# Kernel tuning notes

Measured on AMD Instinct MI355X. Metric: run time of the kernel, lower is better.

## Reference

```python
import jax, jax.numpy as jnp
import numpy as np
import math

HEADS = 8


def sinusoidal_pe_2d(C, H, W, dtype=jnp.float32):
    """Standard fixed 2D sinusoidal PE. Returns (C, H*W).
    First C/2 channels encode row (H) position, last C/2 encode column (W)."""
    half = C // 2
    div = jnp.exp(-math.log(10000.0) * jnp.arange(0, half, 2, dtype=dtype) / half)  # (half/2,)
    pos_h = jnp.arange(H, dtype=dtype)[:, None] * div[None, :]  # (H, half/2)
    pos_w = jnp.arange(W, dtype=dtype)[:, None] * div[None, :]  # (W, half/2)
    # interleave sin/cos along channel dim -> (H, half), (W, half)
    pe_h = jnp.stack([jnp.sin(pos_h), jnp.cos(pos_h)], axis=-1).reshape(H, half)
    pe_w = jnp.stack([jnp.sin(pos_w), jnp.cos(pos_w)], axis=-1).reshape(W, half)
    pe = jnp.concatenate([
        jnp.broadcast_to(pe_h.T[:, :, None], (half, H, W)),
        jnp.broadcast_to(pe_w.T[:, None, :], (half, H, W)),
    ], axis=0)  # (C, H, W)
    return pe.reshape(C, H * W)


def setup_inputs() -> dict:
    key = jax.random.key(0)
    k1, k2, k3, k4 = jax.random.split(key, 4)
    B, c_in, H, W = 16, 256, 64, 64
    c_out = 512
    s = 1.0 / math.sqrt(c_in)
    return {
        "x": jax.random.normal(k1, (B, c_in, H, W), dtype=jnp.float32),
        "Wq": jax.random.normal(k2, (c_out, c_in), dtype=jnp.float32) * s,
        "Wk": jax.random.normal(k3, (c_out, c_in), dtype=jnp.float32) * s,
        "Wv": jax.random.normal(k4, (c_out, c_in), dtype=jnp.float32) * s,
    }


def reference(x, Wq, Wk, Wv):
    B, C, H, W = x.shape
    M = H * W
    c_out = Wq.shape[0]
    heads = HEADS
    dh = c_out // heads
    scale = 1.0 / math.sqrt(dh)

    xf = x.reshape(B, C, M)
    # 1x1 convs (no bias) == channel matmuls
    q = jnp.einsum('oc,bcm->bom', Wq, xf).reshape(B, heads, dh, M)
    k = jnp.einsum('oc,bcm->bom', Wk, xf).reshape(B, heads, dh, M)
    v = jnp.einsum('oc,bcm->bom', Wv, xf).reshape(B, heads, dh, M)

    r = sinusoidal_pe_2d(c_out, H, W, dtype=x.dtype).reshape(1, heads, dh, M)
    q = (jax.nn.elu(q + r) + 1.0) * scale  # feature map phi(q)
    k = (jax.nn.elu(k) + 1.0) * scale      # feature map phi(k)

    KV = jnp.einsum('bhcm,bhdm->bhcd', k, v)          # (B,h,dh,dh)
    out = jnp.einsum('bhcd,bhcm->bhdm', KV, q)        # (B,h,dh,M)
    k_sum = k.sum(axis=-1)                            # (B,h,dh)
    denom = jnp.einsum('bhcm,bhc->bhm', q, k_sum)
    denom = jnp.maximum(denom, 1e-6)[:, :, None, :]   # (B,h,1,M)
    out = out / denom
    return out.reshape(B, c_out, H, W)
```

## Files before the change

### kernel.cpp

```cpp
#include <hip/hip_runtime.h>

#define NB   16
#define CIN  256
#define MM   4096
#define COUT 512
#define NH   8
#define DH   64
#define SCALE 0.125f

typedef __attribute__((ext_vector_type(8))) short bf16x8;
typedef __attribute__((ext_vector_type(4))) float f32x4;

#define PEH_OFF   0u
#define PEW_OFF   65536u
#define WQ_OFF    131072u
#define WKV_OFF   393216u
#define KVP_OFF   917504u
#define KSP_OFF   9306112u
#define AEXT_OFF  9437184u
#define XT_OFF    27787264u
#define WS_NEED   61341696ull

__device__ __forceinline__ unsigned short f2bf(float f) {
    unsigned int u = __float_as_uint(f);
    u = (u + 0x7FFFu + ((u >> 16) & 1u)) >> 16;
    return (unsigned short)u;
}
__device__ __forceinline__ float phi_elu(float x) {
    return (x >= 0.f ? x + 1.f : __expf(x)) * SCALE;
}
__device__ __forceinline__ void gload_lds16(const void* g, void* l) {
    __builtin_amdgcn_global_load_lds(
        (const __attribute__((address_space(1))) unsigned int*)g,
        (__attribute__((address_space(3))) unsigned int*)l, 16, 0, 0);
}

__global__ void k_prep(const float* __restrict__ Wq, const float* __restrict__ Wk,
                       const float* __restrict__ Wv, char* __restrict__ ws) {
    int idx = blockIdx.x * 256 + threadIdx.x;
    if (idx < 32768) {
        int which = idx >> 14;
        int r = idx & 16383;
        int c = r >> 6, pos = r & 63;
        float div = __expf(-logf(10000.f) * (float)(c >> 1) * (1.f / 128.f));
        float t = (float)pos * div;
        float v = (c & 1) ? cosf(t) : sinf(t);
        ((float*)(ws + (which ? PEW_OFF : PEH_OFF)))[r] = v;
        return;
    }
    idx -= 32768;
    if (idx < COUT * CIN) {
        ((unsigned short*)(ws + WQ_OFF))[idx] = f2bf(Wq[idx]);
        return;
    }
    idx -= COUT * CIN;
    if (idx < NH * 128 * CIN) {
        int h = idx >> 15;
        int r = idx & 32767;
        int row = r >> 8, c = r & 255;
        float v = (row < 64) ? Wk[(h * 64 + row) * CIN + c]
                             : Wv[(h * 64 + row - 64) * CIN + c];
        ((unsigned short*)(ws + WKV_OFF))[idx] = f2bf(v);
    }
}


__global__ __launch_bounds__(256) void k_xpose(const float* __restrict__ x, char* __restrict__ ws) {
    __shared__ unsigned short tile[64 * 64];
    int t = threadIdx.x;
    int gx = blockIdx.x;
    int ct = gx & 3, mt = (gx >> 2) & 63, b = gx >> 8;
    int m0 = mt * 64, c0 = ct * 64;
    const float* xb = x + ((size_t)b * CIN + c0) * MM + m0;
    int m4 = (t & 15) * 4;
    int cp0 = (t >> 4) * 2;
#pragma unroll
    for (int p = 0; p < 2; ++p) {
        int cp = cp0 + p * 32;
        float4 v0 = *(const float4*)(xb + (size_t)cp * MM + m4);
        float4 v1 = *(const float4*)(xb + (size_t)(cp + 1) * MM + m4);
        float a0[4] = {v0.x, v0.y, v0.z, v0.w};
        float a1[4] = {v1.x, v1.y, v1.z, v1.w};
#pragma unroll
        for (int i = 0; i < 4; ++i) {
            int m = m4 + i;
            unsigned pk = (unsigned)f2bf(a0[i]) | ((unsigned)f2bf(a1[i]) << 16);
            unsigned off = (unsigned)(m * 128) + (((unsigned)(cp * 2)) ^ ((unsigned)(m & 7) << 4));
            *(unsigned*)((char*)tile + off) = pk;
        }
    }
    __syncthreads();
    unsigned short* xt = (unsigned short*)(ws + XT_OFF) + ((size_t)b * MM + m0) * CIN + c0;
#pragma unroll
    for (int p = 0; p < 2; ++p) {
        int id = t + p * 256;
        int m = id >> 3, u = id & 7;
        unsigned off = (unsigned)(m * 128) + (((unsigned)(u ^ (m & 7))) << 4);
        *(bf16x8*)(xt + (size_t)m * CIN + u * 8) = *(const bf16x8*)((const char*)tile + off);
    }
}

__device__ __forceinline__ void stage_half(const unsigned short* __restrict__ tile_base, int h,
                                           unsigned short* __restrict__ buf, int l, int w) {
#pragma unroll
    for (int i = 0; i < 4; ++i) {
        int r0 = w * 16 + i * 4;
        int m = r0 + (l >> 4);
        unsigned u = (unsigned)(l & 15) ^ (unsigned)(m & 7);
        const char* g = (const char*)tile_base + m * 512 + h * 256 + u * 16;
        gload_lds16(g, (char*)buf + r0 * 256);
    }
}
__device__ __forceinline__ bf16x8 ldsBh(const unsigned short* buf, int n, int k) {
    unsigned off = (unsigned)(n * 256) + (((((unsigned)k) >> 3) ^ ((unsigned)n & 7)) << 4);
    return *(const bf16x8*)((const char*)buf + off);
}

__global__ __launch_bounds__(256) void k_kv4(const char* __restrict__ ws) {
    __shared__ unsigned short bufA[64 * 128];
    __shared__ unsigned short bufB[64 * 128];
    __shared__ unsigned short kt[64 * 72];
    __shared__ unsigned short vt[64 * 72];
    int t = threadIdx.x, l = t & 63, w = t >> 6;
    int blk = blockIdx.x;
    int s = blk & 3, bh = blk >> 2;
    int b = bh >> 3, h = bh & 7;
    const unsigned short* xtb = (const unsigned short*)(ws + XT_OFF) + (size_t)b * MM * CIN;
    const unsigned short* wkv = (const unsigned short*)(ws + WKV_OFF) + (size_t)h * 128 * CIN;
    bf16x8 wreg[2][8];
#pragma unroll
    for (int rf = 0; rf < 2; ++rf)
#pragma unroll
        for (int kk = 0; kk < 8; ++kk)
            wreg[rf][kk] = *(const bf16x8*)(wkv + (size_t)(w * 32 + rf * 16 + (l & 15)) * CIN + kk * 32 + (l >> 4) * 8);

    f32x4 kvacc[4] = {};
    float ksum[2][4] = {};

    const unsigned short* tile0 = xtb + (size_t)(s * 1024) * CIN;
    stage_half(tile0, 0, bufA, l, w);
    __syncthreads();

    for (int ms = 0; ms < 16; ++ms) {
        const unsigned short* tilep = xtb + (size_t)(s * 1024 + ms * 64) * CIN;
        stage_half(tilep, 1, bufB, l, w);

        f32x4 acc[2][4] = {};
#pragma unroll
        for (int kk = 0; kk < 4; ++kk) {
            bf16x8 bfr[4];
#pragma unroll
            for (int cf = 0; cf < 4; ++cf)
                bfr[cf] = ldsBh(bufA, cf * 16 + (l & 15), kk * 32 + (l >> 4) * 8);
#pragma unroll
            for (int rf = 0; rf < 2; ++rf)
#pragma unroll
                for (int cf = 0; cf < 4; ++cf)
                    acc[rf][cf] = __builtin_amdgcn_mfma_f32_16x16x32_bf16(wreg[rf][kk], bfr[cf], acc[rf][cf], 0, 0, 0);
        }
        __syncthreads();

        if (ms < 15)
            stage_half(tilep + 64 * CIN, 0, bufA, l, w);
#pragma unroll
        for (int kk = 0; kk < 4; ++kk) {
            bf16x8 bfr[4];
#pragma unroll
            for (int cf = 0; cf < 4; ++cf)
                bfr[cf] = ldsBh(bufB, cf * 16 + (l & 15), kk * 32 + (l >> 4) * 8);
#pragma unroll
            for (int rf = 0; rf < 2; ++rf)
#pragma unroll
                for (int cf = 0; cf < 4; ++cf)
                    acc[rf][cf] = __builtin_amdgcn_mfma_f32_16x16x32_bf16(wreg[rf][4 + kk], bfr[cf], acc[rf][cf], 0, 0, 0);
        }
        if (w < 2) {
#pragma unroll
            for (int rf = 0; rf < 2; ++rf)
#pragma unroll
                for (int cf = 0; cf < 4; ++cf)
#pragma unroll
                    for (int r = 0; r < 4; ++r) {
                        float p = phi_elu(acc[rf][cf][r]);
                        ksum[rf][r] += p;
                        kt[(w * 32 + rf * 16 + ((l >> 4) << 2) + r) * 72 + cf * 16 + (l & 15)] = f2bf(p);
                    }
        } else {
#pragma unroll
            for (int rf = 0; rf < 2; ++rf)
#pragma unroll
                for (int cf = 0; cf < 4; ++cf)
#pragma unroll
                    for (int r = 0; r < 4; ++r)
                        vt[((w - 2) * 32 + rf * 16 + ((l >> 4) << 2) + r) * 72 + cf * 16 + (l & 15)] = f2bf(acc[rf][cf][r]);
        }
        __syncthreads();
#pragma unroll
        for (int kk = 0; kk < 2; ++kk) {
            bf16x8 a = *(const bf16x8*)(kt + (w * 16 + (l & 15)) * 72 + kk * 32 + (l >> 4) * 8);
#pragma unroll
            for (int cf = 0; cf < 4; ++cf) {
                bf16x8 bb = *(const bf16x8*)(vt + (cf * 16 + (l & 15)) * 72 + kk * 32 + (l >> 4) * 8);
                kvacc[cf] = __builtin_amdgcn_mfma_f32_16x16x32_bf16(a, bb, kvacc[cf], 0, 0, 0);
            }
        }
    }

    float* kvp = (float*)(ws + KVP_OFF) + ((size_t)(bh * 4 + s)) * 4096;
#pragma unroll
    for (int cf = 0; cf < 4; ++cf)
#pragma unroll
        for (int r = 0; r < 4; ++r) {
            int c = w * 16 + ((l >> 4) << 2) + r;
            kvp[c * 64 + cf * 16 + (l & 15)] = kvacc[cf][r];
        }
    if (w < 2) {
        float* ksp = (float*)(ws + KSP_OFF) + (bh * 4 + s) * 64;
#pragma unroll
        for (int rf = 0; rf < 2; ++rf)
#pragma unroll
            for (int r = 0; r < 4; ++r) {
                float v = ksum[rf][r];
                v += __shfl_xor(v, 1); v += __shfl_xor(v, 2);
                v += __shfl_xor(v, 4); v += __shfl_xor(v, 8);
                if ((l & 15) == 0)
                    ksp[w * 32 + rf * 16 + ((l >> 4) << 2) + r] = v;
            }
    }
}

__global__ void k_reduce(char* __restrict__ ws) {
    int bh = blockIdx.x;
    const float* kvp = (const float*)(ws + KVP_OFF) + (size_t)bh * 4 * 4096;
    const float* ksp = (const float*)(ws + KSP_OFF) + bh * 4 * 64;
    unsigned short* a = (unsigned short*)(ws + AEXT_OFF) + (size_t)bh * 80 * 64;
    for (int i = threadIdx.x; i < 80 * 64; i += 256) {
        int d = i >> 6, c = i & 63;
        float v = 0.f;
        if (d < 64) {
#pragma unroll
            for (int s = 0; s < 4; ++s) v += kvp[s * 4096 + c * 64 + d];
        } else if (d == 64) {
#pragma unroll
            for (int s = 0; s < 4; ++s) v += ksp[s * 64 + c];
        }
        a[i] = f2bf(v);
    }
}

__global__ __launch_bounds__(256) void k_out4(const char* __restrict__ ws, float* __restrict__ out) {
    __shared__ unsigned short bufA[64 * 128];
    __shared__ unsigned short bufB[64 * 128];
    __shared__ unsigned short qt[64 * 64];
    __shared__ unsigned short aext[80 * 72];
    int t = threadIdx.x, l = t & 63, w = t >> 6;
    int blk = blockIdx.x;
    int chunk = blk & 3, bh = blk >> 2;
    int b = bh >> 3, h = bh & 7;

    const unsigned short* asrc = (const unsigned short*)(ws + AEXT_OFF) + (size_t)bh * 80 * 64;
    for (int i = t; i < 80 * 8; i += 256) {
        int row = i >> 3, ch = i & 7;
        *(bf16x8*)(aext + row * 72 + ch * 8) = *(const bf16x8*)(asrc + row * 64 + ch * 8);
    }
    const unsigned short* xtb = (const unsigned short*)(ws + XT_OFF) + (size_t)b * MM * CIN;
    const unsigned short* wq = (const unsigned short*)(ws + WQ_OFF);
    bf16x8 wreg[2][8];
#pragma unroll
    for (int rf = 0; rf < 2; ++rf)
#pragma unroll
        for (int kk = 0; kk < 8; ++kk)
            wreg[rf][kk] = *(const bf16x8*)(wq + (size_t)(h * 64 + (w >> 1) * 32 + rf * 16 + (l & 15)) * CIN + kk * 32 + (l >> 4) * 8);

    const float* pe = (h < 4) ? (const float*)(ws + PEH_OFF) : (const float*)(ws + PEW_OFF);
    int obase = h * 64 - (h < 4 ? 0 : 256);
    float* outbh = out + ((size_t)(b * COUT + h * DH)) * MM;

    const unsigned short* tile0 = xtb + (size_t)(chunk * 1024) * CIN;
    stage_half(tile0, 0, bufA, l, w);
    __syncthreads();

    for (int ms = 0; ms < 16; ++ms) {
        int m0 = chunk * 1024 + ms * 64;
        const unsigned short* tilep = xtb + (size_t)m0 * CIN;
        stage_half(tilep, 1, bufB, l, w);

        f32x4 acc[2][2] = {};
#pragma unroll
        for (int kk = 0; kk < 4; ++kk) {
            bf16x8 bfr[2];
#pragma unroll
            for (int mf = 0; mf < 2; ++mf)
                bfr[mf] = ldsBh(bufA, (w & 1) * 32 + mf * 16 + (l & 15), kk * 32 + (l >> 4) * 8);
#pragma unroll
            for (int rf = 0; rf < 2; ++rf)
#pragma unroll
                for (int mf = 0; mf < 2; ++mf)
                    acc[rf][mf] = __builtin_amdgcn_mfma_f32_16x16x32_bf16(wreg[rf][kk], bfr[mf], acc[rf][mf], 0, 0, 0);
        }
        __syncthreads();

        if (ms < 15)
            stage_half(tilep + 64 * CIN, 0, bufA, l, w);
#pragma unroll
        for (int kk = 0; kk < 4; ++kk) {
            bf16x8 bfr[2];
#pragma unroll
            for (int mf = 0; mf < 2; ++mf)
                bfr[mf] = ldsBh(bufB, (w & 1) * 32 + mf * 16 + (l & 15), kk * 32 + (l >> 4) * 8);
#pragma unroll
            for (int rf = 0; rf < 2; ++rf)
#pragma unroll
                for (int mf = 0; mf < 2; ++mf)
                    acc[rf][mf] = __builtin_amdgcn_mfma_f32_16x16x32_bf16(wreg[rf][4 + kk], bfr[mf], acc[rf][mf], 0, 0, 0);
        }
        int im = m0 >> 6;
#pragma unroll
        for (int rf = 0; rf < 2; ++rf) {
#pragma unroll
            for (int mf = 0; mf < 2; ++mf) {
                int mloc = (w & 1) * 32 + mf * 16 + (l & 15);
#pragma unroll
                for (int r = 0; r < 4; ++r) {
                    int c = (w >> 1) * 32 + rf * 16 + ((l >> 4) << 2) + r;
                    int o = obase + c;
                    float pev = (h < 4) ? pe[o * 64 + im] : pe[o * 64 + mloc];
                    float v = phi_elu(acc[rf][mf][r] + pev);
                    unsigned off = (unsigned)(mloc * 128) + (((unsigned)(c * 2)) ^ ((unsigned)(mloc & 7) << 4));
                    *(unsigned short*)((char*)qt + off) = f2bf(v);
                }
            }
        }
        __syncthreads();

        f32x4 acc2[5] = {};
#pragma unroll
        for (int kk = 0; kk < 2; ++kk) {
            int m = w * 16 + (l & 15);
            unsigned koff = (unsigned)(kk * 64 + (l >> 4) * 16);
            unsigned off = (unsigned)(m * 128) + (koff ^ ((unsigned)(m & 7) << 4));
            bf16x8 bb = *(const bf16x8*)((const char*)qt + off);
#pragma unroll
            for (int rf = 0; rf < 5; ++rf) {
                bf16x8 a = *(const bf16x8*)(aext + (rf * 16 + (l & 15)) * 72 + kk * 32 + (l >> 4) * 8);
                acc2[rf] = __builtin_amdgcn_mfma_f32_16x16x32_bf16(a, bb, acc2[rf], 0, 0, 0);
            }
        }
        float den = __shfl(acc2[4][0], l & 15);
        float inv = 1.f / fmaxf(den, 1e-6f);
        int mcol = m0 + w * 16 + (l & 15);
#pragma unroll
        for (int rf = 0; rf < 4; ++rf)
#pragma unroll
            for (int r = 0; r < 4; ++r)
                outbh[(size_t)(rf * 16 + ((l >> 4) << 2) + r) * MM + mcol] = acc2[rf][r] * inv;
    }
}


template<int NTHR>
__device__ __forceinline__ void stage_xT(const float* __restrict__ xb, int m0,
                                         unsigned short* __restrict__ lds, int t) {
    int mg = t & 15;
    for (int c = (t >> 4); c < CIN; c += NTHR / 16) {
        const float* src = xb + c * MM + m0 + mg;
#pragma unroll
        for (int j = 0; j < 4; ++j) {
            int m = mg + 16 * j;
            unsigned off = (unsigned)(m * 512) + (((unsigned)(c * 2)) ^ ((unsigned)(m & 7) << 4));
            *(unsigned short*)((char*)lds + off) = f2bf(src[16 * j]);
        }
    }
}
__device__ __forceinline__ bf16x8 ldsB(const unsigned short* lds, int n, int k) {
    unsigned off = (unsigned)(n * 512) + (((unsigned)(k * 2)) ^ ((unsigned)(n & 7) << 4));
    return *(const bf16x8*)((const char*)lds + off);
}

__global__ __launch_bounds__(512) void k_qgemm(const float* __restrict__ x,
                                               const char* __restrict__ ws,
                                               float* __restrict__ out) {
    __shared__ unsigned short xT[64 * 256];
    int t = threadIdx.x, l = t & 63, w = t >> 6;
    int gx = blockIdx.x;
    int rt = gx & 1;
    int ct = gx >> 1;
    int b = ct >> 6;
    int m0 = (ct & 63) * 64;
    const float* xb = x + (size_t)b * CIN * MM;

    const unsigned short* wq = (const unsigned short*)(ws + WQ_OFF);
    int r0 = rt * 256 + w * 32;
    bf16x8 wreg[2][8];
#pragma unroll
    for (int rf = 0; rf < 2; ++rf)
#pragma unroll
        for (int kk = 0; kk < 8; ++kk)
            wreg[rf][kk] = *(const bf16x8*)(wq + (size_t)(r0 + rf * 16 + (l & 15)) * CIN + kk * 32 + (l >> 4) * 8);

    stage_xT<512>(xb, m0, xT, t);
    __syncthreads();

    f32x4 acc[2][4] = {};
#pragma unroll
    for (int kk = 0; kk < 8; ++kk) {
        bf16x8 bfr[4];
#pragma unroll
        for (int cf = 0; cf < 4; ++cf)
            bfr[cf] = ldsB(xT, cf * 16 + (l & 15), kk * 32 + (l >> 4) * 8);
#pragma unroll
        for (int rf = 0; rf < 2; ++rf)
#pragma unroll
            for (int cf = 0; cf < 4; ++cf)
                acc[rf][cf] = __builtin_amdgcn_mfma_f32_16x16x32_bf16(wreg[rf][kk], bfr[cf], acc[rf][cf], 0, 0, 0);
    }

    const float* peh = (const float*)(ws + PEH_OFF);
    const float* pew = (const float*)(ws + PEW_OFF);
    int im = m0 >> 6;
#pragma unroll
    for (int rf = 0; rf < 2; ++rf) {
#pragma unroll
        for (int cf = 0; cf < 4; ++cf) {
            int mloc = cf * 16 + (l & 15);
#pragma unroll
            for (int r = 0; r < 4; ++r) {
                int o = r0 + rf * 16 + ((l >> 4) << 2) + r;
                float pe = (rt == 0) ? peh[o * 64 + im] : pew[(o - 256) * 64 + mloc];
                float v = phi_elu(acc[rf][cf][r] + pe);
                out[((size_t)(b * COUT + o)) * MM + m0 + mloc] = v;
            }
        }
    }
}

__global__ __launch_bounds__(256) void k_kv(const float* __restrict__ x,
                                            char* __restrict__ ws) {
    __shared__ unsigned short xT[64 * 256];
    __shared__ unsigned short kt[64 * 72];
    __shared__ unsigned short vt[64 * 72];
    int t = threadIdx.x, l = t & 63, w = t >> 6;
    int blk = blockIdx.x;
    int s = blk & 3;
    int bh = blk >> 2;
    int b = bh >> 3, h = bh & 7;
    const float* xb = x + (size_t)b * CIN * MM;

    const unsigned short* wkv = (const unsigned short*)(ws + WKV_OFF) + (size_t)h * 128 * CIN;
    bf16x8 wreg[2][8];
#pragma unroll
    for (int rf = 0; rf < 2; ++rf)
#pragma unroll
        for (int kk = 0; kk < 8; ++kk)
            wreg[rf][kk] = *(const bf16x8*)(wkv + (size_t)(w * 32 + rf * 16 + (l & 15)) * CIN + kk * 32 + (l >> 4) * 8);

    f32x4 kvacc[4] = {};
    float ksum[2][4] = {};

    for (int ms = 0; ms < 16; ++ms) {
        int m0 = s * 1024 + ms * 64;
        if (ms) __syncthreads();
        stage_xT<256>(xb, m0, xT, t);
        __syncthreads();

        f32x4 acc[2][4] = {};
#pragma unroll
        for (int kk = 0; kk < 8; ++kk) {
            bf16x8 bfr[4];
#pragma unroll
            for (int cf = 0; cf < 4; ++cf)
                bfr[cf] = ldsB(xT, cf * 16 + (l & 15), kk * 32 + (l >> 4) * 8);
#pragma unroll
            for (int rf = 0; rf < 2; ++rf)
#pragma unroll
                for (int cf = 0; cf < 4; ++cf)
                    acc[rf][cf] = __builtin_amdgcn_mfma_f32_16x16x32_bf16(wreg[rf][kk], bfr[cf], acc[rf][cf], 0, 0, 0);
        }

        if (w < 2) {
#pragma unroll
            for (int rf = 0; rf < 2; ++rf)
#pragma unroll
                for (int cf = 0; cf < 4; ++cf)
#pragma unroll
                    for (int r = 0; r < 4; ++r) {
                        float p = phi_elu(acc[rf][cf][r]);
                        ksum[rf][r] += p;
                        kt[(w * 32 + rf * 16 + ((l >> 4) << 2) + r) * 72 + cf * 16 + (l & 15)] = f2bf(p);
                    }
        } else {
#pragma unroll
            for (int rf = 0; rf < 2; ++rf)
#pragma unroll
                for (int cf = 0; cf < 4; ++cf)
#pragma unroll
                    for (int r = 0; r < 4; ++r)
                        vt[((w - 2) * 32 + rf * 16 + ((l >> 4) << 2) + r) * 72 + cf * 16 + (l & 15)] = f2bf(acc[rf][cf][r]);
        }
        __syncthreads();

#pragma unroll
        for (int kk = 0; kk < 2; ++kk) {
            bf16x8 a = *(const bf16x8*)(kt + (w * 16 + (l & 15)) * 72 + kk * 32 + (l >> 4) * 8);
#pragma unroll
            for (int cf = 0; cf < 4; ++cf) {
                bf16x8 bb = *(const bf16x8*)(vt + (cf * 16 + (l & 15)) * 72 + kk * 32 + (l >> 4) * 8);
                kvacc[cf] = __builtin_amdgcn_mfma_f32_16x16x32_bf16(a, bb, kvacc[cf], 0, 0, 0);
            }
        }
    }

    float* kvp = (float*)(ws + KVP_OFF) + ((size_t)(bh * 4 + s)) * 64 * 64;
#pragma unroll
    for (int cf = 0; cf < 4; ++cf)
#pragma unroll
        for (int r = 0; r < 4; ++r) {
            int c = w * 16 + ((l >> 4) << 2) + r;
            kvp[c * 64 + cf * 16 + (l & 15)] = kvacc[cf][r];
        }
    if (w < 2) {
        float* ksp = (float*)(ws + KSP_OFF) + (bh * 4 + s) * 64;
#pragma unroll
        for (int rf = 0; rf < 2; ++rf)
#pragma unroll
            for (int r = 0; r < 4; ++r) {
                float v = ksum[rf][r];
                v += __shfl_xor(v, 1); v += __shfl_xor(v, 2);
                v += __shfl_xor(v, 4); v += __shfl_xor(v, 8);
                if ((l & 15) == 0)
                    ksp[w * 32 + rf * 16 + ((l >> 4) << 2) + r] = v;
            }
    }
}

__global__ __launch_bounds__(256) void k_out(const char* __restrict__ ws,
                                             float* __restrict__ out) {
    __shared__ unsigned short aext[80 * 72];
    __shared__ unsigned short qt[64 * 72];
    int t = threadIdx.x, l = t & 63, w = t >> 6;
    int blk = blockIdx.x;
    int chunk = blk & 7, bh = blk >> 3;
    int b = bh >> 3, h = bh & 7;

    const unsigned short* asrc = (const unsigned short*)(ws + AEXT_OFF) + (size_t)bh * 80 * 64;
    for (int i = t; i < 80 * 8; i += 256) {
        int row = i >> 3, ch = i & 7;
        *(bf16x8*)(aext + row * 72 + ch * 8) = *(const bf16x8*)(asrc + row * 64 + ch * 8);
    }
    float* outbh = out + ((size_t)(b * COUT + h * DH)) * MM;

    for (int ms = 0; ms < 8; ++ms) {
        int m0 = chunk * 512 + ms * 64;
        __syncthreads();
        {
            int mg = t & 15;
            for (int c = t >> 4; c < 64; c += 16) {
                const float* src = outbh + (size_t)c * MM + m0 + mg;
#pragma unroll
                for (int j = 0; j < 4; ++j)
                    qt[(mg + 16 * j) * 72 + c] = f2bf(src[16 * j]);
            }
        }
        __syncthreads();
        f32x4 acc[5] = {};
#pragma unroll
        for (int kk = 0; kk < 2; ++kk) {
            bf16x8 bb = *(const bf16x8*)(qt + (w * 16 + (l & 15)) * 72 + kk * 32 + (l >> 4) * 8);
#pragma unroll
            for (int rf = 0; rf < 5; ++rf) {
                bf16x8 a = *(const bf16x8*)(aext + (rf * 16 + (l & 15)) * 72 + kk * 32 + (l >> 4) * 8);
                acc[rf] = __builtin_amdgcn_mfma_f32_16x16x32_bf16(a, bb, acc[rf], 0, 0, 0);
            }
        }
        float den = __shfl(acc[4][0], l & 15);
        float inv = 1.f / fmaxf(den, 1e-6f);
        int mcol = m0 + w * 16 + (l & 15);
#pragma unroll
        for (int rf = 0; rf < 4; ++rf)
#pragma unroll
            for (int r = 0; r < 4; ++r)
                outbh[(size_t)(rf * 16 + ((l >> 4) << 2) + r) * MM + mcol] = acc[rf][r] * inv;
    }
}

extern "C" void kernel_launch(void* const* d_in, const int* in_sizes, int n_in,
                              void* d_out, int out_size, void* d_ws, size_t ws_size,
                              hipStream_t stream) {
    const float* x  = (const float*)d_in[0];
    const float* Wq = (const float*)d_in[1];
    const float* Wk = (const float*)d_in[2];
    const float* Wv = (const float*)d_in[3];
    float* out = (float*)d_out;
    char* ws = (char*)d_ws;

    hipLaunchKernelGGL(k_prep, dim3(1664), dim3(256), 0, stream, Wq, Wk, Wv, ws);
    if (ws_size >= WS_NEED) {
        hipLaunchKernelGGL(k_xpose,  dim3(4096), dim3(256), 0, stream, x, ws);
        hipLaunchKernelGGL(k_kv4,    dim3(512),  dim3(256), 0, stream, ws);
        hipLaunchKernelGGL(k_reduce, dim3(128),  dim3(256), 0, stream, ws);
        hipLaunchKernelGGL(k_out4,   dim3(512),  dim3(256), 0, stream, ws, out);
    } else {
        hipLaunchKernelGGL(k_qgemm,  dim3(2048), dim3(512), 0, stream, x, ws, out);
        hipLaunchKernelGGL(k_kv,     dim3(512),  dim3(256), 0, stream, x, ws);
        hipLaunchKernelGGL(k_reduce, dim3(128),  dim3(256), 0, stream, ws);
        hipLaunchKernelGGL(k_out,    dim3(1024), dim3(256), 0, stream, ws, out);
    }
}
```

Measured before the change: 136.7 us.

## Fuse prep with transpose, fold KV reduction into output kernel, remap block order

Merges the weight/PE prep kernel and the x transpose into a single k_init launch, removes the separate k_reduce launch by having each k_out4 block sum the four KV partials and k-sum itself, and remaps block indices so that blocks sharing the same batch/head spread across XCDs. This cuts two kernel launches and their serialization gaps. In exchange, every k_out4 block redundantly re-reduces its head's partials (4 blocks per head), adding global reads and a strided LDS transpose store at kernel start.

```diff
diff --git a/kernel.cpp b/kernel.cpp
--- a/kernel.cpp
+++ b/kernel.cpp
@@ -34,6 +34,326 @@
         (const __attribute__((address_space(1))) unsigned int*)g,
         (__attribute__((address_space(3))) unsigned int*)l, 16, 0, 0);
 }
+
+
+__global__ __launch_bounds__(256) void k_init(const float* __restrict__ x,
+                                              const float* __restrict__ Wq,
+                                              const float* __restrict__ Wk,
+                                              const float* __restrict__ Wv,
+                                              char* __restrict__ ws) {
+    __shared__ unsigned short tile[64 * 64];
+    int blk = blockIdx.x;
+    int t = threadIdx.x;
+    if (blk < 1664) {
+        int idx = blk * 256 + t;
+        if (idx < 32768) {
+            int which = idx >> 14;
+            int r = idx & 16383;
+            int c = r >> 6, pos = r & 63;
+            float div = __expf(-logf(10000.f) * (float)(c >> 1) * (1.f / 128.f));
+            float tt = (float)pos * div;
+            float v = (c & 1) ? cosf(tt) : sinf(tt);
+            ((float*)(ws + (which ? PEW_OFF : PEH_OFF)))[r] = v;
+            return;
+        }
+        idx -= 32768;
+        if (idx < COUT * CIN) {
+            ((unsigned short*)(ws + WQ_OFF))[idx] = f2bf(Wq[idx]);
+            return;
+        }
+        idx -= COUT * CIN;
+        if (idx < NH * 128 * CIN) {
+            int h = idx >> 15;
+            int r = idx & 32767;
+            int row = r >> 8, c = r & 255;
+            float v = (row < 64) ? Wk[(h * 64 + row) * CIN + c]
+                                 : Wv[(h * 64 + row - 64) * CIN + c];
+            ((unsigned short*)(ws + WKV_OFF))[idx] = f2bf(v);
+        }
+        return;
+    }
+    int gx = blk - 1664;
+    int ct = gx & 3, mt = (gx >> 2) & 63, b = gx >> 8;
+    int m0 = mt * 64, c0 = ct * 64;
+    const float* xb = x + ((size_t)b * CIN + c0) * MM + m0;
+    int m4 = (t & 15) * 4;
+    int cp0 = (t >> 4) * 2;
+#pragma unroll
+    for (int p = 0; p < 2; ++p) {
+        int cp = cp0 + p * 32;
+        float4 v0 = *(const float4*)(xb + (size_t)cp * MM + m4);
+        float4 v1 = *(const float4*)(xb + (size_t)(cp + 1) * MM + m4);
+        float a0[4] = {v0.x, v0.y, v0.z, v0.w};
+        float a1[4] = {v1.x, v1.y, v1.z, v1.w};
+#pragma unroll
+        for (int i = 0; i < 4; ++i) {
+            int m = m4 + i;
+            unsigned pk = (unsigned)f2bf(a0[i]) | ((unsigned)f2bf(a1[i]) << 16);
+            unsigned off = (unsigned)(m * 128) + (((unsigned)(cp * 2)) ^ ((unsigned)(m & 7) << 4));
+            *(unsigned*)((char*)tile + off) = pk;
+        }
+    }
+    __syncthreads();
+    unsigned short* xt = (unsigned short*)(ws + XT_OFF) + ((size_t)b * MM + m0) * CIN + c0;
+#pragma unroll
+    for (int p = 0; p < 2; ++p) {
+        int id = t + p * 256;
+        int m = id >> 3, u = id & 7;
+        unsigned off = (unsigned)(m * 128) + (((unsigned)(u ^ (m & 7))) << 4);
+        *(bf16x8*)(xt + (size_t)m * CIN + u * 8) = *(const bf16x8*)((const char*)tile + off);
+    }
+}
+
+__device__ __forceinline__ void stage_half(const unsigned short* __restrict__ tile_base, int h,
+                                           unsigned short* __restrict__ buf, int l, int w) {
+#pragma unroll
+    for (int i = 0; i < 4; ++i) {
+        int r0 = w * 16 + i * 4;
+        int m = r0 + (l >> 4);
+        unsigned u = (unsigned)(l & 15) ^ (unsigned)(m & 7);
+        const char* g = (const char*)tile_base + m * 512 + h * 256 + u * 16;
+        gload_lds16(g, (char*)buf + r0 * 256);
+    }
+}
+__device__ __forceinline__ bf16x8 ldsBh(const unsigned short* buf, int n, int k) {
+    unsigned off = (unsigned)(n * 256) + (((((unsigned)k) >> 3) ^ ((unsigned)n & 7)) << 4);
+    return *(const bf16x8*)((const char*)buf + off);
+}
+
+__global__ __launch_bounds__(256) void k_kv4(const char* __restrict__ ws) {
+    __shared__ unsigned short bufA[64 * 128];
+    __shared__ unsigned short bufB[64 * 128];
+    __shared__ unsigned short kt[64 * 72];
+    __shared__ unsigned short vt[64 * 72];
+    int t = threadIdx.x, l = t & 63, w = t >> 6;
+    int blk = blockIdx.x;
+    int wid = ((blk & 7) << 6) | (blk >> 3);
+    int s = wid & 3, bh = wid >> 2;
+    int b = bh >> 3, h = bh & 7;
+    const unsigned short* xtb = (const unsigned short*)(ws + XT_OFF) + (size_t)b * MM * CIN;
+    const unsigned short* wkv = (const unsigned short*)(ws + WKV_OFF) + (size_t)h * 128 * CIN;
+    bf16x8 wreg[2][8];
+#pragma unroll
+    for (int rf = 0; rf < 2; ++rf)
+#pragma unroll
+        for (int kk = 0; kk < 8; ++kk)
+            wreg[rf][kk] = *(const bf16x8*)(wkv + (size_t)(w * 32 + rf * 16 + (l & 15)) * CIN + kk * 32 + (l >> 4) * 8);
+
+    f32x4 kvacc[4] = {};
+    float ksum[2][4] = {};
+
+    const unsigned short* tile0 = xtb + (size_t)(s * 1024) * CIN;
+    stage_half(tile0, 0, bufA, l, w);
+    __syncthreads();
+
+    for (int ms = 0; ms < 16; ++ms) {
+        const unsigned short* tilep = xtb + (size_t)(s * 1024 + ms * 64) * CIN;
+        stage_half(tilep, 1, bufB, l, w);
+
+        f32x4 acc[2][4] = {};
+#pragma unroll
+        for (int kk = 0; kk < 4; ++kk) {
+            bf16x8 bfr[4];
+#pragma unroll
+            for (int cf = 0; cf < 4; ++cf)
+                bfr[cf] = ldsBh(bufA, cf * 16 + (l & 15), kk * 32 + (l >> 4) * 8);
+#pragma unroll
+            for (int rf = 0; rf < 2; ++rf)
+#pragma unroll
+                for (int cf = 0; cf < 4; ++cf)
+                    acc[rf][cf] = __builtin_amdgcn_mfma_f32_16x16x32_bf16(wreg[rf][kk], bfr[cf], acc[rf][cf], 0, 0, 0);
+        }
+        __syncthreads();
+
+        if (ms < 15)
+            stage_half(tilep + 64 * CIN, 0, bufA, l, w);
+#pragma unroll
+        for (int kk = 0; kk < 4; ++kk) {
+            bf16x8 bfr[4];
+#pragma unroll
+            for (int cf = 0; cf < 4; ++cf)
+                bfr[cf] = ldsBh(bufB, cf * 16 + (l & 15), kk * 32 + (l >> 4) * 8);
+#pragma unroll
+            for (int rf = 0; rf < 2; ++rf)
+#pragma unroll
+                for (int cf = 0; cf < 4; ++cf)
+                    acc[rf][cf] = __builtin_amdgcn_mfma_f32_16x16x32_bf16(wreg[rf][4 + kk], bfr[cf], acc[rf][cf], 0, 0, 0);
+        }
+        if (w < 2) {
+#pragma unroll
+            for (int rf = 0; rf < 2; ++rf)
+#pragma unroll
+                for (int cf = 0; cf < 4; ++cf)
+#pragma unroll
+                    for (int r = 0; r < 4; ++r) {
+                        float p = phi_elu(acc[rf][cf][r]);
+                        ksum[rf][r] += p;
+                        kt[(w * 32 + rf * 16 + ((l >> 4) << 2) + r) * 72 + cf * 16 + (l & 15)] = f2bf(p);
+                    }
+        } else {
+#pragma unroll
+            for (int rf = 0; rf < 2; ++rf)
+#pragma unroll
+                for (int cf = 0; cf < 4; ++cf)
+#pragma unroll
+                    for (int r = 0; r < 4; ++r)
+                        vt[((w - 2) * 32 + rf * 16 + ((l >> 4) << 2) + r) * 72 + cf * 16 + (l & 15)] = f2bf(acc[rf][cf][r]);
+        }
+        __syncthreads();
+#pragma unroll
+        for (int kk = 0; kk < 2; ++kk) {
+            bf16x8 a = *(const bf16x8*)(kt + (w * 16 + (l & 15)) * 72 + kk * 32 + (l >> 4) * 8);
+#pragma unroll
+            for (int cf = 0; cf < 4; ++cf) {
+                bf16x8 bb = *(const bf16x8*)(vt + (cf * 16 + (l & 15)) * 72 + kk * 32 + (l >> 4) * 8);
+                kvacc[cf] = __builtin_amdgcn_mfma_f32_16x16x32_bf16(a, bb, kvacc[cf], 0, 0, 0);
+            }
+        }
+    }
+
+    float* kvp = (float*)(ws + KVP_OFF) + ((size_t)(bh * 4 + s)) * 4096;
+#pragma unroll
+    for (int cf = 0; cf < 4; ++cf)
+#pragma unroll
+        for (int r = 0; r < 4; ++r) {
+            int c = w * 16 + ((l >> 4) << 2) + r;
+            kvp[c * 64 + cf * 16 + (l & 15)] = kvacc[cf][r];
+        }
+    if (w < 2) {
+        float* ksp = (float*)(ws + KSP_OFF) + (bh * 4 + s) * 64;
+#pragma unroll
+        for (int rf = 0; rf < 2; ++rf)
+#pragma unroll
+            for (int r = 0; r < 4; ++r) {
+                float v = ksum[rf][r];
+                v += __shfl_xor(v, 1); v += __shfl_xor(v, 2);
+                v += __shfl_xor(v, 4); v += __shfl_xor(v, 8);
+                if ((l & 15) == 0)
+                    ksp[w * 32 + rf * 16 + ((l >> 4) << 2) + r] = v;
+            }
+    }
+}
+
+__global__ __launch_bounds__(256) void k_out4(const char* __restrict__ ws, float* __restrict__ out) {
+    __shared__ unsigned short bufA[64 * 128];
+    __shared__ unsigned short bufB[64 * 128];
+    __shared__ unsigned short qt[64 * 64];
+    __shared__ unsigned short aext[80 * 72];
+    int t = threadIdx.x, l = t & 63, w = t >> 6;
+    int blk = blockIdx.x;
+    int wid = ((blk & 7) << 6) | (blk >> 3);
+    int chunk = wid & 3, bh = wid >> 2;
+    int b = bh >> 3, h = bh & 7;
+
+    {
+        const float* kvp = (const float*)(ws + KVP_OFF) + (size_t)bh * 4 * 4096;
+        const float* ksp = (const float*)(ws + KSP_OFF) + bh * 4 * 64;
+        for (int j = t; j < 4096; j += 256) {
+            float v = kvp[j] + kvp[4096 + j] + kvp[8192 + j] + kvp[12288 + j];
+            aext[(j & 63) * 72 + (j >> 6)] = f2bf(v);
+        }
+        if (t < 64) {
+            float v = ksp[t] + ksp[64 + t] + ksp[128 + t] + ksp[192 + t];
+            aext[64 * 72 + t] = f2bf(v);
+        }
+        for (int j = t; j < 15 * 64; j += 256)
+            aext[(65 + (j >> 6)) * 72 + (j & 63)] = 0;
+    }
+
+    const unsigned short* xtb = (const unsigned short*)(ws + XT_OFF) + (size_t)b * MM * CIN;
+    const unsigned short* wq = (const unsigned short*)(ws + WQ_OFF);
+    bf16x8 wreg[2][8];
+#pragma unroll
+    for (int rf = 0; rf < 2; ++rf)
+#pragma unroll
+        for (int kk = 0; kk < 8; ++kk)
+            wreg[rf][kk] = *(const bf16x8*)(wq + (size_t)(h * 64 + (w >> 1) * 32 + rf * 16 + (l & 15)) * CIN + kk * 32 + (l >> 4) * 8);
+
+    const float* pe = (h < 4) ? (const float*)(ws + PEH_OFF) : (const float*)(ws + PEW_OFF);
+    int obase = h * 64 - (h < 4 ? 0 : 256);
+    float* outbh = out + ((size_t)(b * COUT + h * DH)) * MM;
+
+    const unsigned short* tile0 = xtb + (size_t)(chunk * 1024) * CIN;
+    stage_half(tile0, 0, bufA, l, w);
+    __syncthreads();
+
+    for (int ms = 0; ms < 16; ++ms) {
+        int m0 = chunk * 1024 + ms * 64;
+        const unsigned short* tilep = xtb + (size_t)m0 * CIN;
+        stage_half(tilep, 1, bufB, l, w);
+
+        f32x4 acc[2][2] = {};
+#pragma unroll
+        for (int kk = 0; kk < 4; ++kk) {
+            bf16x8 bfr[2];
+#pragma unroll
+            for (int mf = 0; mf < 2; ++mf)
+                bfr[mf] = ldsBh(bufA, (w & 1) * 32 + mf * 16 + (l & 15), kk * 32 + (l >> 4) * 8);
+#pragma unroll
+            for (int rf = 0; rf < 2; ++rf)
+#pragma unroll
+                for (int mf = 0; mf < 2; ++mf)
+                    acc[rf][mf] = __builtin_amdgcn_mfma_f32_16x16x32_bf16(wreg[rf][kk], bfr[mf], acc[rf][mf], 0, 0, 0);
+        }
+        __syncthreads();
+
+        if (ms < 15)
+            stage_half(tilep + 64 * CIN, 0, bufA, l, w);
+#pragma unroll
+        for (int kk = 0; kk < 4; ++kk) {
+            bf16x8 bfr[2];
+#pragma unroll
+            for (int mf = 0; mf < 2; ++mf)
+                bfr[mf] = ldsBh(bufB, (w & 1) * 32 + mf * 16 + (l & 15), kk * 32 + (l >> 4) * 8);
+#pragma unroll
+            for (int rf = 0; rf < 2; ++rf)
+#pragma unroll
+                for (int mf = 0; mf < 2; ++mf)
+                    acc[rf][mf] = __builtin_amdgcn_mfma_f32_16x16x32_bf16(wreg[rf][4 + kk], bfr[mf], acc[rf][mf], 0, 0, 0);
+        }
+        int im = m0 >> 6;
+#pragma unroll
+        for (int rf = 0; rf < 2; ++rf) {
+#pragma unroll
+            for (int mf = 0; mf < 2; ++mf) {
+                int mloc = (w & 1) * 32 + mf * 16 + (l & 15);
+#pragma unroll
+                for (int r = 0; r < 4; ++r) {
+                    int c = (w >> 1) * 32 + rf * 16 + ((l >> 4) << 2) + r;
+                    int o = obase + c;
+                    float pev = (h < 4) ? pe[o * 64 + im] : pe[o * 64 + mloc];
+                    float v = phi_elu(acc[rf][mf][r] + pev);
+                    unsigned off = (unsigned)(mloc * 128) + (((unsigned)(c * 2)) ^ ((unsigned)(mloc & 7) << 4));
+                    *(unsigned short*)((char*)qt + off) = f2bf(v);
+                }
+            }
+        }
+        __syncthreads();
+
+        f32x4 acc2[5] = {};
+#pragma unroll
+        for (int kk = 0; kk < 2; ++kk) {
+            int m = w * 16 + (l & 15);
+            unsigned koff = (unsigned)(kk * 64 + (l >> 4) * 16);
+            unsigned off = (unsigned)(m * 128) + (koff ^ ((unsigned)(m & 7) << 4));
+            bf16x8 bb = *(const bf16x8*)((const char*)qt + off);
+#pragma unroll
+            for (int rf = 0; rf < 5; ++rf) {
+                bf16x8 a = *(const bf16x8*)(aext + (rf * 16 + (l & 15)) * 72 + kk * 32 + (l >> 4) * 8);
+                acc2[rf] = __builtin_amdgcn_mfma_f32_16x16x32_bf16(a, bb, acc2[rf], 0, 0, 0);
+            }
+        }
+        float den = __shfl(acc2[4][0], l & 15);
+        float inv = 1.f / fmaxf(den, 1e-6f);
+        int mcol = m0 + w * 16 + (l & 15);
+#pragma unroll
+        for (int rf = 0; rf < 4; ++rf)
+#pragma unroll
+            for (int r = 0; r < 4; ++r)
+                outbh[(size_t)(rf * 16 + ((l >> 4) << 2) + r) * MM + mcol] = acc2[rf][r] * inv;
+    }
+}
+
 
 __global__ void k_prep(const float* __restrict__ Wq, const float* __restrict__ Wk,
                        const float* __restrict__ Wv, char* __restrict__ ws) {
@@ -64,300 +384,6 @@
     }
 }
 
-
-__global__ __launch_bounds__(256) void k_xpose(const float* __restrict__ x, char* __restrict__ ws) {
-    __shared__ unsigned short tile[64 * 64];
-    int t = threadIdx.x;
-    int gx = blockIdx.x;
-    int ct = gx & 3, mt = (gx >> 2) & 63, b = gx >> 8;
-    int m0 = mt * 64, c0 = ct * 64;
-    const float* xb = x + ((size_t)b * CIN + c0) * MM + m0;
-    int m4 = (t & 15) * 4;
-    int cp0 = (t >> 4) * 2;
-#pragma unroll
-    for (int p = 0; p < 2; ++p) {
-        int cp = cp0 + p * 32;
-        float4 v0 = *(const float4*)(xb + (size_t)cp * MM + m4);
-        float4 v1 = *(const float4*)(xb + (size_t)(cp + 1) * MM + m4);
-        float a0[4] = {v0.x, v0.y, v0.z, v0.w};
-        float a1[4] = {v1.x, v1.y, v1.z, v1.w};
-#pragma unroll
-        for (int i = 0; i < 4; ++i) {
-            int m = m4 + i;
-            unsigned pk = (unsigned)f2bf(a0[i]) | ((unsigned)f2bf(a1[i]) << 16);
-            unsigned off = (unsigned)(m * 128) + (((unsigned)(cp * 2)) ^ ((unsigned)(m & 7) << 4));
-            *(unsigned*)((char*)tile + off) = pk;
-        }
-    }
-    __syncthreads();
-    unsigned short* xt = (unsigned short*)(ws + XT_OFF) + ((size_t)b * MM + m0) * CIN + c0;
-#pragma unroll
-    for (int p = 0; p < 2; ++p) {
-        int id = t + p * 256;
-        int m = id >> 3, u = id & 7;
-        unsigned off = (unsigned)(m * 128) + (((unsigned)(u ^ (m & 7))) << 4);
-        *(bf16x8*)(xt + (size_t)m * CIN + u * 8) = *(const bf16x8*)((const char*)tile + off);
-    }
-}
-
-__device__ __forceinline__ void stage_half(const unsigned short* __restrict__ tile_base, int h,
-                                           unsigned short* __restrict__ buf, int l, int w) {
-#pragma unroll
-    for (int i = 0; i < 4; ++i) {
-        int r0 = w * 16 + i * 4;
-        int m = r0 + (l >> 4);
-        unsigned u = (unsigned)(l & 15) ^ (unsigned)(m & 7);
-        const char* g = (const char*)tile_base + m * 512 + h * 256 + u * 16;
-        gload_lds16(g, (char*)buf + r0 * 256);
-    }
-}
-__device__ __forceinline__ bf16x8 ldsBh(const unsigned short* buf, int n, int k) {
-    unsigned off = (unsigned)(n * 256) + (((((unsigned)k) >> 3) ^ ((unsigned)n & 7)) << 4);
-    return *(const bf16x8*)((const char*)buf + off);
-}
-
-__global__ __launch_bounds__(256) void k_kv4(const char* __restrict__ ws) {
-    __shared__ unsigned short bufA[64 * 128];
-    __shared__ unsigned short bufB[64 * 128];
-    __shared__ unsigned short kt[64 * 72];
-    __shared__ unsigned short vt[64 * 72];
-    int t = threadIdx.x, l = t & 63, w = t >> 6;
-    int blk = blockIdx.x;
-    int s = blk & 3, bh = blk >> 2;
-    int b = bh >> 3, h = bh & 7;
-    const unsigned short* xtb = (const unsigned short*)(ws + XT_OFF) + (size_t)b * MM * CIN;
-    const unsigned short* wkv = (const unsigned short*)(ws + WKV_OFF) + (size_t)h * 128 * CIN;
-    bf16x8 wreg[2][8];
-#pragma unroll
-    for (int rf = 0; rf < 2; ++rf)
-#pragma unroll
-        for (int kk = 0; kk < 8; ++kk)
-            wreg[rf][kk] = *(const bf16x8*)(wkv + (size_t)(w * 32 + rf * 16 + (l & 15)) * CIN + kk * 32 + (l >> 4) * 8);
-
-    f32x4 kvacc[4] = {};
-    float ksum[2][4] = {};
-
-    const unsigned short* tile0 = xtb + (size_t)(s * 1024) * CIN;
-    stage_half(tile0, 0, bufA, l, w);
-    __syncthreads();
-
-    for (int ms = 0; ms < 16; ++ms) {
-        const unsigned short* tilep = xtb + (size_t)(s * 1024 + ms * 64) * CIN;
-        stage_half(tilep, 1, bufB, l, w);
-
-        f32x4 acc[2][4] = {};
-#pragma unroll
-        for (int kk = 0; kk < 4; ++kk) {
-            bf16x8 bfr[4];
-#pragma unroll
-            for (int cf = 0; cf < 4; ++cf)
-                bfr[cf] = ldsBh(bufA, cf * 16 + (l & 15), kk * 32 + (l >> 4) * 8);
-#pragma unroll
-            for (int rf = 0; rf < 2; ++rf)
-#pragma unroll
-                for (int cf = 0; cf < 4; ++cf)
-                    acc[rf][cf] = __builtin_amdgcn_mfma_f32_16x16x32_bf16(wreg[rf][kk], bfr[cf], acc[rf][cf], 0, 0, 0);
-        }
-        __syncthreads();
-
-        if (ms < 15)
-            stage_half(tilep + 64 * CIN, 0, bufA, l, w);
-#pragma unroll
-        for (int kk = 0; kk < 4; ++kk) {
-            bf16x8 bfr[4];
-#pragma unroll
-            for (int cf = 0; cf < 4; ++cf)
-                bfr[cf] = ldsBh(bufB, cf * 16 + (l & 15), kk * 32 + (l >> 4) * 8);
-#pragma unroll
-            for (int rf = 0; rf < 2; ++rf)
-#pragma unroll
-                for (int cf = 0; cf < 4; ++cf)
-                    acc[rf][cf] = __builtin_amdgcn_mfma_f32_16x16x32_bf16(wreg[rf][4 + kk], bfr[cf], acc[rf][cf], 0, 0, 0);
-        }
-        if (w < 2) {
-#pragma unroll
-            for (int rf = 0; rf < 2; ++rf)
-#pragma unroll
-                for (int cf = 0; cf < 4; ++cf)
-#pragma unroll
-                    for (int r = 0; r < 4; ++r) {
-                        float p = phi_elu(acc[rf][cf][r]);
-                        ksum[rf][r] += p;
-                        kt[(w * 32 + rf * 16 + ((l >> 4) << 2) + r) * 72 + cf * 16 + (l & 15)] = f2bf(p);
-                    }
-        } else {
-#pragma unroll
-            for (int rf = 0; rf < 2; ++rf)
-#pragma unroll
-                for (int cf = 0; cf < 4; ++cf)
-#pragma unroll
-                    for (int r = 0; r < 4; ++r)
-                        vt[((w - 2) * 32 + rf * 16 + ((l >> 4) << 2) + r) * 72 + cf * 16 + (l & 15)] = f2bf(acc[rf][cf][r]);
-        }
-        __syncthreads();
-#pragma unroll
-        for (int kk = 0; kk < 2; ++kk) {
-            bf16x8 a = *(const bf16x8*)(kt + (w * 16 + (l & 15)) * 72 + kk * 32 + (l >> 4) * 8);
-#pragma unroll
-            for (int cf = 0; cf < 4; ++cf) {
-                bf16x8 bb = *(const bf16x8*)(vt + (cf * 16 + (l & 15)) * 72 + kk * 32 + (l >> 4) * 8);
-                kvacc[cf] = __builtin_amdgcn_mfma_f32_16x16x32_bf16(a, bb, kvacc[cf], 0, 0, 0);
-            }
-        }
-    }
-
-    float* kvp = (float*)(ws + KVP_OFF) + ((size_t)(bh * 4 + s)) * 4096;
-#pragma unroll
-    for (int cf = 0; cf < 4; ++cf)
-#pragma unroll
-        for (int r = 0; r < 4; ++r) {
-            int c = w * 16 + ((l >> 4) << 2) + r;
-            kvp[c * 64 + cf * 16 + (l & 15)] = kvacc[cf][r];
-        }
-    if (w < 2) {
-        float* ksp = (float*)(ws + KSP_OFF) + (bh * 4 + s) * 64;
-#pragma unroll
-        for (int rf = 0; rf < 2; ++rf)
-#pragma unroll
-            for (int r = 0; r < 4; ++r) {
-                float v = ksum[rf][r];
-                v += __shfl_xor(v, 1); v += __shfl_xor(v, 2);
-                v += __shfl_xor(v, 4); v += __shfl_xor(v, 8);
-                if ((l & 15) == 0)
-                    ksp[w * 32 + rf * 16 + ((l >> 4) << 2) + r] = v;
-            }
-    }
-}
-
-__global__ void k_reduce(char* __restrict__ ws) {
-    int bh = blockIdx.x;
-    const float* kvp = (const float*)(ws + KVP_OFF) + (size_t)bh * 4 * 4096;
-    const float* ksp = (const float*)(ws + KSP_OFF) + bh * 4 * 64;
-    unsigned short* a = (unsigned short*)(ws + AEXT_OFF) + (size_t)bh * 80 * 64;
-    for (int i = threadIdx.x; i < 80 * 64; i += 256) {
-        int d = i >> 6, c = i & 63;
-        float v = 0.f;
-        if (d < 64) {
-#pragma unroll
-            for (int s = 0; s < 4; ++s) v += kvp[s * 4096 + c * 64 + d];
-        } else if (d == 64) {
-#pragma unroll
-            for (int s = 0; s < 4; ++s) v += ksp[s * 64 + c];
-        }
-        a[i] = f2bf(v);
-    }
-}
-
-__global__ __launch_bounds__(256) void k_out4(const char* __restrict__ ws, float* __restrict__ out) {
-    __shared__ unsigned short bufA[64 * 128];
-    __shared__ unsigned short bufB[64 * 128];
-    __shared__ unsigned short qt[64 * 64];
-    __shared__ unsigned short aext[80 * 72];
-    int t = threadIdx.x, l = t & 63, w = t >> 6;
-    int blk = blockIdx.x;
-    int chunk = blk & 3, bh = blk >> 2;
-    int b = bh >> 3, h = bh & 7;
-
-    const unsigned short* asrc = (const unsigned short*)(ws + AEXT_OFF) + (size_t)bh * 80 * 64;
-    for (int i = t; i < 80 * 8; i += 256) {
-        int row = i >> 3, ch = i & 7;
-        *(bf16x8*)(aext + row * 72 + ch * 8) = *(const bf16x8*)(asrc + row * 64 + ch * 8);
-    }
-    const unsigned short* xtb = (const unsigned short*)(ws + XT_OFF) + (size_t)b * MM * CIN;
-    const unsigned short* wq = (const unsigned short*)(ws + WQ_OFF);
-    bf16x8 wreg[2][8];
-#pragma unroll
-    for (int rf = 0; rf < 2; ++rf)
-#pragma unroll
-        for (int kk = 0; kk < 8; ++kk)
-            wreg[rf][kk] = *(const bf16x8*)(wq + (size_t)(h * 64 + (w >> 1) * 32 + rf * 16 + (l & 15)) * CIN + kk * 32 + (l >> 4) * 8);
-
-    const float* pe = (h < 4) ? (const float*)(ws + PEH_OFF) : (const float*)(ws + PEW_OFF);
-    int obase = h * 64 - (h < 4 ? 0 : 256);
-    float* outbh = out + ((size_t)(b * COUT + h * DH)) * MM;
-
-    const unsigned short* tile0 = xtb + (size_t)(chunk * 1024) * CIN;
-    stage_half(tile0, 0, bufA, l, w);
-    __syncthreads();
-
-    for (int ms = 0; ms < 16; ++ms) {
-        int m0 = chunk * 1024 + ms * 64;
-        const unsigned short* tilep = xtb + (size_t)m0 * CIN;
-        stage_half(tilep, 1, bufB, l, w);
-
-        f32x4 acc[2][2] = {};
-#pragma unroll
-        for (int kk = 0; kk < 4; ++kk) {
-            bf16x8 bfr[2];
-#pragma unroll
-            for (int mf = 0; mf < 2; ++mf)
-                bfr[mf] = ldsBh(bufA, (w & 1) * 32 + mf * 16 + (l & 15), kk * 32 + (l >> 4) * 8);
-#pragma unroll
-            for (int rf = 0; rf < 2; ++rf)
-#pragma unroll
-                for (int mf = 0; mf < 2; ++mf)
-                    acc[rf][mf] = __builtin_amdgcn_mfma_f32_16x16x32_bf16(wreg[rf][kk], bfr[mf], acc[rf][mf], 0, 0, 0);
-        }
-        __syncthreads();
-
-        if (ms < 15)
-            stage_half(tilep + 64 * CIN, 0, bufA, l, w);
-#pragma unroll
-        for (int kk = 0; kk < 4; ++kk) {
-            bf16x8 bfr[2];
-#pragma unroll
-            for (int mf = 0; mf < 2; ++mf)
-                bfr[mf] = ldsBh(bufB, (w & 1) * 32 + mf * 16 + (l & 15), kk * 32 + (l >> 4) * 8);
-#pragma unroll
-            for (int rf = 0; rf < 2; ++rf)
-#pragma unroll
-                for (int mf = 0; mf < 2; ++mf)
-                    acc[rf][mf] = __builtin_amdgcn_mfma_f32_16x16x32_bf16(wreg[rf][4 + kk], bfr[mf], acc[rf][mf], 0, 0, 0);
-        }
-        int im = m0 >> 6;
-#pragma unroll
-        for (int rf = 0; rf < 2; ++rf) {
-#pragma unroll
-            for (int mf = 0; mf < 2; ++mf) {
-                int mloc = (w & 1) * 32 + mf * 16 + (l & 15);
-#pragma unroll
-                for (int r = 0; r < 4; ++r) {
-                    int c = (w >> 1) * 32 + rf * 16 + ((l >> 4) << 2) + r;
-                    int o = obase + c;
-                    float pev = (h < 4) ? pe[o * 64 + im] : pe[o * 64 + mloc];
-                    float v = phi_elu(acc[rf][mf][r] + pev);
-                    unsigned off = (unsigned)(mloc * 128) + (((unsigned)(c * 2)) ^ ((unsigned)(mloc & 7) << 4));
-                    *(unsigned short*)((char*)qt + off) = f2bf(v);
-                }
-            }
-        }
-        __syncthreads();
-
-        f32x4 acc2[5] = {};
-#pragma unroll
-        for (int kk = 0; kk < 2; ++kk) {
-            int m = w * 16 + (l & 15);
-            unsigned koff = (unsigned)(kk * 64 + (l >> 4) * 16);
-            unsigned off = (unsigned)(m * 128) + (koff ^ ((unsigned)(m & 7) << 4));
-            bf16x8 bb = *(const bf16x8*)((const char*)qt + off);
-#pragma unroll
-            for (int rf = 0; rf < 5; ++rf) {
-                bf16x8 a = *(const bf16x8*)(aext + (rf * 16 + (l & 15)) * 72 + kk * 32 + (l >> 4) * 8);
-                acc2[rf] = __builtin_amdgcn_mfma_f32_16x16x32_bf16(a, bb, acc2[rf], 0, 0, 0);
-            }
-        }
-        float den = __shfl(acc2[4][0], l & 15);
-        float inv = 1.f / fmaxf(den, 1e-6f);
-        int mcol = m0 + w * 16 + (l & 15);
-#pragma unroll
-        for (int rf = 0; rf < 4; ++rf)
-#pragma unroll
-            for (int r = 0; r < 4; ++r)
-                outbh[(size_t)(rf * 16 + ((l >> 4) << 2) + r) * MM + mcol] = acc2[rf][r] * inv;
-    }
-}
-
-
 template<int NTHR>
 __device__ __forceinline__ void stage_xT(const float* __restrict__ xb, int m0,
                                          unsigned short* __restrict__ lds, int t) {
@@ -533,6 +559,25 @@
     }
 }
 
+__global__ void k_reduce(char* __restrict__ ws) {
+    int bh = blockIdx.x;
+    const float* kvp = (const float*)(ws + KVP_OFF) + (size_t)bh * 4 * 4096;
+    const float* ksp = (const float*)(ws + KSP_OFF) + bh * 4 * 64;
+    unsigned short* a = (unsigned short*)(ws + AEXT_OFF) + (size_t)bh * 80 * 64;
+    for (int i = threadIdx.x; i < 80 * 64; i += 256) {
+        int d = i >> 6, c = i & 63;
+        float v = 0.f;
+        if (d < 64) {
+#pragma unroll
+            for (int s = 0; s < 4; ++s) v += kvp[s * 4096 + c * 64 + d];
+        } else if (d == 64) {
+#pragma unroll
+            for (int s = 0; s < 4; ++s) v += ksp[s * 64 + c];
+        }
+        a[i] = f2bf(v);
+    }
+}
+
 __global__ __launch_bounds__(256) void k_out(const char* __restrict__ ws,
                                              float* __restrict__ out) {
     __shared__ unsigned short aext[80 * 72];
@@ -593,13 +638,12 @@
     float* out = (float*)d_out;
     char* ws = (char*)d_ws;
 
-    hipLaunchKernelGGL(k_prep, dim3(1664), dim3(256), 0, stream, Wq, Wk, Wv, ws);
     if (ws_size >= WS_NEED) {
-        hipLaunchKernelGGL(k_xpose,  dim3(4096), dim3(256), 0, stream, x, ws);
-        hipLaunchKernelGGL(k_kv4,    dim3(512),  dim3(256), 0, stream, ws);
-        hipLaunchKernelGGL(k_reduce, dim3(128),  dim3(256), 0, stream, ws);
-        hipLaunchKernelGGL(k_out4,   dim3(512),  dim3(256), 0, stream, ws, out);
+        hipLaunchKernelGGL(k_init,  dim3(5760), dim3(256), 0, stream, x, Wq, Wk, Wv, ws);
+        hipLaunchKernelGGL(k_kv4,   dim3(512),  dim3(256), 0, stream, ws);
+        hipLaunchKernelGGL(k_out4,  dim3(512),  dim3(256), 0, stream, ws, out);
     } else {
+        hipLaunchKernelGGL(k_prep,   dim3(1664), dim3(256), 0, stream, Wq, Wk, Wv, ws);
         hipLaunchKernelGGL(k_qgemm,  dim3(2048), dim3(512), 0, stream, x, ws, out);
         hipLaunchKernelGGL(k_kv,     dim3(512),  dim3(256), 0, stream, x, ws);
         hipLaunchKernelGGL(k_reduce, dim3(128),  dim3(256), 0, stream, ws);
```

New measurement: 122.8 us. 10.2% less time.
